# Optimization experiments

Hardware: AMD Instinct MI355X
Metric: run time of the kernel (lower is better)

The kernel has to match this reference:

```python
import jax, jax.numpy as jnp
import numpy as np

B, N, IN_F = 16, 1024, 256
HEADS, OUT_F = 4, 64
NEG_SLOPE = 0.2
CLAMP_MIN = -1e9
MASK_VAL = -9e15


def setup_inputs() -> dict:
    key = jax.random.key(0)
    k1, k2, k3, k4 = jax.random.split(key, 4)
    x = jax.random.normal(k1, (B, N, IN_F), dtype=jnp.float32)
    adj = jax.random.randint(k2, (B, N, N), 0, 2, dtype=jnp.int32)
    # Linear weight, stored as (in, heads*out) so y = x @ W (xavier-uniform scale)
    lim_w = float(np.sqrt(6.0 / (IN_F + HEADS * OUT_F)))
    W = jax.random.uniform(k3, (IN_F, HEADS * OUT_F), dtype=jnp.float32,
                           minval=-lim_w, maxval=lim_w)
    lim_a = float(np.sqrt(6.0 / (2 * OUT_F + HEADS)))
    a = jax.random.uniform(k4, (2 * OUT_F, HEADS), dtype=jnp.float32,
                           minval=-lim_a, maxval=lim_a)
    return {"x": x, "adj": adj, "W": W, "a": a}


def reference(x, adj, W, a):
    Bs, Ns, _ = x.shape
    # Projection: (B,N,H,D)
    h = (x @ W).reshape(Bs, Ns, HEADS, OUT_F)
    # cat([h_i, h_j]) . a == h_i . a_src + h_j . a_dst  (exact same math, no O(N^2*2D) tensor)
    a_src, a_dst = a[:OUT_F], a[OUT_F:]          # each (D, H)
    s_src = jnp.einsum('bnhd,dh->bnh', h, a_src)  # score contribution of node i
    s_dst = jnp.einsum('bnhd,dh->bnh', h, a_dst)  # score contribution of node j
    e = jax.nn.leaky_relu(s_src[:, :, None, :] + s_dst[:, None, :, :],
                          negative_slope=NEG_SLOPE)  # (B,N,N,H)
    # match original: subtract unmasked row max, clamp, then mask, then softmax over j
    e = e - jnp.max(e, axis=2, keepdims=True)
    e = jnp.maximum(e, CLAMP_MIN)
    att = jnp.where(adj[..., None] > 0, e, MASK_VAL)
    att = jax.nn.softmax(att, axis=2)
    h_prime = jnp.einsum('bijh,bjhd->bihd', att, h)  # (B,N,H,D)
    return h_prime.reshape(Bs, Ns, HEADS * OUT_F)
```

## Files before the change

kernel.cpp:

```cpp
#include <hip/hip_runtime.h>
#include <hip/hip_bf16.h>

#define B_   16
#define N_   1024
#define INF_ 256
#define NH_  4
#define HD_  256
#define L2E  1.4426950408889634f

typedef __attribute__((ext_vector_type(8))) short short8;
typedef __attribute__((ext_vector_type(4))) float f32x4;

__device__ __forceinline__ float bf2f(unsigned short u) {
    union { unsigned int i; float f; } v; v.i = ((unsigned int)u) << 16; return v.f;
}
__device__ __forceinline__ unsigned short f2bf(float f) {
    union { float f; unsigned int i; } v; v.f = f;
    unsigned int x = v.i;
    return (unsigned short)((x + 0x7fffu + ((x >> 16) & 1u)) >> 16);
}

__global__ __launch_bounds__(256) void k_prep(const int* __restrict__ adj,
                                              const float* __restrict__ W,
                                              unsigned int* __restrict__ pb,
                                              unsigned short* __restrict__ wswz)
{
    int bx = blockIdx.x, t = threadIdx.x;
    if (bx < 2048) {
        int wave = t >> 6, lane = t & 63;
        int row = bx * 8 + wave * 2 + (lane >> 5);
        int w   = lane & 31;
        const int4* ar = (const int4*)(adj + ((long)row << 10) + w * 32);
        unsigned int u = 0;
        #pragma unroll
        for (int k = 0; k < 8; k++) {
            int4 a = ar[k];
            u |= ((unsigned)a.x) << (4 * k);
            u |= ((unsigned)a.y) << (4 * k + 1);
            u |= ((unsigned)a.z) << (4 * k + 2);
            u |= ((unsigned)a.w) << (4 * k + 3);
        }
        pb[((long)row << 5) + w] = u;
    } else {
        int slot = (bx - 2048) * 256 + t;
        int kstep = slot >> 10;
        int nt    = (slot >> 6) & 15;
        int lane  = slot & 63;
        int k0 = kstep * 32 + (lane >> 4) * 8;
        int n  = nt * 16 + (lane & 15);
        ushort4 o0, o1;
        o0.x = f2bf(W[(k0 + 0) * HD_ + n]);
        o0.y = f2bf(W[(k0 + 1) * HD_ + n]);
        o0.z = f2bf(W[(k0 + 2) * HD_ + n]);
        o0.w = f2bf(W[(k0 + 3) * HD_ + n]);
        o1.x = f2bf(W[(k0 + 4) * HD_ + n]);
        o1.y = f2bf(W[(k0 + 5) * HD_ + n]);
        o1.z = f2bf(W[(k0 + 6) * HD_ + n]);
        o1.w = f2bf(W[(k0 + 7) * HD_ + n]);
        *(ushort4*)&wswz[(long)slot * 8]     = o0;
        *(ushort4*)&wswz[(long)slot * 8 + 4] = o1;
    }
}

__global__ __launch_bounds__(256) void k_gemm_h(
    const float* __restrict__ x, const float* __restrict__ a,
    const unsigned short* __restrict__ wswz,
    unsigned short* __restrict__ hswz,
    float* __restrict__ ssrc, float* __restrict__ sdst)
{
    __shared__ unsigned short xls[16][264];
    int t = threadIdx.x;
    int blk = blockIdx.x;
    int row0 = blk * 16;
    int b  = blk >> 6;
    int n0 = row0 & 1023;

    {
        int sr = t >> 4, sc = (t & 15) * 16;
        const float* xp = x + (long)(row0 + sr) * INF_ + sc;
        float4 v0 = ((const float4*)xp)[0];
        float4 v1 = ((const float4*)xp)[1];
        float4 v2 = ((const float4*)xp)[2];
        float4 v3 = ((const float4*)xp)[3];
        ushort4 u0 = {f2bf(v0.x), f2bf(v0.y), f2bf(v0.z), f2bf(v0.w)};
        ushort4 u1 = {f2bf(v1.x), f2bf(v1.y), f2bf(v1.z), f2bf(v1.w)};
        ushort4 u2 = {f2bf(v2.x), f2bf(v2.y), f2bf(v2.z), f2bf(v2.w)};
        ushort4 u3 = {f2bf(v3.x), f2bf(v3.y), f2bf(v3.z), f2bf(v3.w)};
        *(ushort4*)&xls[sr][sc]      = u0;
        *(ushort4*)&xls[sr][sc + 4]  = u1;
        *(ushort4*)&xls[sr][sc + 8]  = u2;
        *(ushort4*)&xls[sr][sc + 12] = u3;
    }
    __syncthreads();

    int wave = t >> 6, lane = t & 63, quad = lane >> 4, l15 = lane & 15;
    f32x4 acc[4];
    #pragma unroll
    for (int i = 0; i < 4; i++) acc[i] = (f32x4){0.f, 0.f, 0.f, 0.f};

    #pragma unroll
    for (int ks = 0; ks < 8; ks++) {
        short8 af = *(const short8*)&xls[l15][ks * 32 + quad * 8];
        #pragma unroll
        for (int nt = 0; nt < 4; nt++) {
            short8 bf = *(const short8*)(wswz +
                ((long)((ks * 16 + wave * 4 + nt) * 64 + lane)) * 8);
            acc[nt] = __builtin_amdgcn_mfma_f32_16x16x32_bf16(af, bf, acc[nt], 0, 0, 0);
        }
    }

    int q0 = (quad & 1) * 4;
    int qd = ((row0 & 31) + quad * 4) >> 3;
    long bj32 = row0 >> 5;
    #pragma unroll
    for (int nt = 0; nt < 4; nt++) {
        int dg = wave * 4 + nt;
        long idx8 = (bj32 * 16 + dg) * 64 + qd * 16 + l15;
        ushort4 o = {f2bf(acc[nt][0]), f2bf(acc[nt][1]),
                     f2bf(acc[nt][2]), f2bf(acc[nt][3])};
        *(ushort4*)&hswz[idx8 * 8 + q0] = o;
    }

    float as_[4], ad_[4];
    #pragma unroll
    for (int nt = 0; nt < 4; nt++) {
        int d = nt * 16 + l15;
        as_[nt] = a[d * NH_ + wave];
        ad_[nt] = a[(64 + d) * NH_ + wave];
    }
    #pragma unroll
    for (int r = 0; r < 4; r++) {
        float ps = acc[0][r] * as_[0] + acc[1][r] * as_[1]
                 + acc[2][r] * as_[2] + acc[3][r] * as_[3];
        float pd = acc[0][r] * ad_[0] + acc[1][r] * ad_[1]
                 + acc[2][r] * ad_[2] + acc[3][r] * ad_[3];
        #pragma unroll
        for (int m = 1; m < 16; m <<= 1) {
            ps += __shfl_xor(ps, m);
            pd += __shfl_xor(pd, m);
        }
        if (l15 == 0) {
            int row = n0 + quad * 4 + r;
            ssrc[((long)b * NH_ + wave) * N_ + row] = ps * L2E;
            sdst[((long)b * NH_ + wave) * N_ + row] = pd * L2E;
        }
    }
}

__global__ __launch_bounds__(512, 4) void k_attn(
    const unsigned int* __restrict__ pb, const unsigned short* __restrict__ hswz,
    const float* __restrict__ ssrc, const float* __restrict__ sdst,
    float* __restrict__ out)
{
    __shared__ float ss_s[4][32];
    __shared__ float accb[4][2][64][20];

    int t = threadIdx.x;
    int b  = blockIdx.x >> 5, ig = blockIdx.x & 31;
    int i0 = ig * 32;
    int wave = t >> 6, lane = t & 63, quad = lane >> 4, l15 = lane & 15;
    int hh = wave & 3, jh = wave >> 2;

    if (t < 128) {
        int h = t >> 5, i = t & 31;
        ss_s[h][i] = ssrc[((long)(b * NH_ + h)) * N_ + i0 + i];
    }
    __syncthreads();

    float ss0 = ss_s[hh][l15];
    float ss1 = ss_s[hh][16 + l15];
    const float* sdp = sdst + ((long)(b * NH_ + hh)) * N_ + jh * 512;
    long grow0 = ((long)b << 10) + i0 + l15;
    const unsigned int* pb0 = pb + (grow0 << 5) + jh * 16;
    const unsigned int* pb1 = pb0 + (16 << 5);

    f32x4 acc0[4], acc1[4], dn0, dn1;
    #pragma unroll
    for (int i = 0; i < 4; i++) {
        acc0[i] = (f32x4){0.f, 0.f, 0.f, 0.f};
        acc1[i] = (f32x4){0.f, 0.f, 0.f, 0.f};
    }
    dn0 = (f32x4){0.f, 0.f, 0.f, 0.f};
    dn1 = (f32x4){0.f, 0.f, 0.f, 0.f};
    short8 ones;
    #pragma unroll
    for (int i = 0; i < 8; i++) ones[i] = (short)0x3F80;

    int shq = quad * 8;

    #pragma unroll 4
    for (int jc = 0; jc < 16; jc++) {
        unsigned int m0 = (pb0[jc] >> shq) & 0xffu;
        unsigned int m1 = (pb1[jc] >> shq) & 0xffu;
        const float* sj = sdp + jc * 32 + quad * 8;
        float4 sA = *(const float4*)sj;
        float4 sB = *(const float4*)(sj + 4);
        float sv[8] = {sA.x, sA.y, sA.z, sA.w, sB.x, sB.y, sB.z, sB.w};

        union { unsigned int u[4]; short8 s; } p0, p1;
        #pragma unroll
        for (int qp = 0; qp < 4; qp++) {
            unsigned int wb[2][2];
            #pragma unroll
            for (int hv = 0; hv < 2; hv++) {
                int q = 2 * qp + hv;
                float e0 = ss0 + sv[q];
                float w0 = __builtin_exp2f(fmaxf(e0, 0.2f * e0));
                w0 = ((m0 >> q) & 1u) ? w0 : 0.f;
                float e1 = ss1 + sv[q];
                float w1 = __builtin_exp2f(fmaxf(e1, 0.2f * e1));
                w1 = ((m1 >> q) & 1u) ? w1 : 0.f;
                wb[0][hv] = __float_as_uint(w0) + 0x8000u;
                wb[1][hv] = __float_as_uint(w1) + 0x8000u;
            }
            p0.u[qp] = (wb[0][1] & 0xffff0000u) | (wb[0][0] >> 16);
            p1.u[qp] = (wb[1][1] & 0xffff0000u) | (wb[1][0] >> 16);
        }

        long s8 = ((long)(b * 32 + jh * 16 + jc)) * 1024;
        #pragma unroll
        for (int idt = 0; idt < 4; idt++) {
            short8 bf = *(const short8*)(hswz + (s8 + (hh * 4 + idt) * 64 + lane) * 8);
            acc0[idt] = __builtin_amdgcn_mfma_f32_16x16x32_bf16(p0.s, bf, acc0[idt], 0, 0, 0);
            acc1[idt] = __builtin_amdgcn_mfma_f32_16x16x32_bf16(p1.s, bf, acc1[idt], 0, 0, 0);
        }
        dn0 = __builtin_amdgcn_mfma_f32_16x16x32_bf16(p0.s, ones, dn0, 0, 0, 0);
        dn1 = __builtin_amdgcn_mfma_f32_16x16x32_bf16(p1.s, ones, dn1, 0, 0, 0);
    }

    if (jh == 1) {
        #pragma unroll
        for (int idt = 0; idt < 4; idt++) {
            *(f32x4*)&accb[hh][0][lane][idt * 4] = acc0[idt];
            *(f32x4*)&accb[hh][1][lane][idt * 4] = acc1[idt];
        }
        *(f32x4*)&accb[hh][0][lane][16] = dn0;
        *(f32x4*)&accb[hh][1][lane][16] = dn1;
    }
    __syncthreads();

    if (jh == 0) {
        f32x4 od0 = *(const f32x4*)&accb[hh][0][lane][16];
        f32x4 od1 = *(const f32x4*)&accb[hh][1][lane][16];
        float inv0[4], inv1[4];
        #pragma unroll
        for (int r = 0; r < 4; r++) {
            inv0[r] = 1.0f / (dn0[r] + od0[r]);
            inv1[r] = 1.0f / (dn1[r] + od1[r]);
        }
        #pragma unroll
        for (int idt = 0; idt < 4; idt++) {
            f32x4 o0 = *(const f32x4*)&accb[hh][0][lane][idt * 4];
            f32x4 o1 = *(const f32x4*)&accb[hh][1][lane][idt * 4];
            int col = hh * 64 + idt * 16 + l15;
            #pragma unroll
            for (int r = 0; r < 4; r++) {
                long row_g = (long)b * N_ + i0 + quad * 4 + r;
                out[row_g * HD_ + col] = (acc0[idt][r] + o0[r]) * inv0[r];
                out[(row_g + 16) * HD_ + col] = (acc1[idt][r] + o1[r]) * inv1[r];
            }
        }
    }
}

extern "C" void kernel_launch(void* const* d_in, const int* in_sizes, int n_in,
                              void* d_out, int out_size, void* d_ws, size_t ws_size,
                              hipStream_t stream) {
    const float* x   = (const float*)d_in[0];
    const int*   adj = (const int*)d_in[1];
    const float* W   = (const float*)d_in[2];
    const float* a   = (const float*)d_in[3];
    float* out = (float*)d_out;

    unsigned int* pb      = (unsigned int*)d_ws;
    unsigned short* hswz  = (unsigned short*)(pb + 524288);
    unsigned short* wswz  = hswz + (long)B_ * N_ * HD_;
    float* ssrc = (float*)(wswz + INF_ * HD_);
    float* sdst = ssrc + (long)B_ * NH_ * N_;

    k_prep<<<2080, 256, 0, stream>>>(adj, W, pb, wswz);
    k_gemm_h<<<1024, 256, 0, stream>>>(x, a, wswz, hswz, ssrc, sdst);
    k_attn<<<512, 512, 0, stream>>>(pb, hswz, ssrc, sdst, out);
}
```

Before: 156.0 us.

## Fuse adjacency bitpacking into attention kernel and halve rows per block

```diff
diff --git a/kernel.cpp b/kernel.cpp
--- a/kernel.cpp
+++ b/kernel.cpp
@@ -20,46 +20,26 @@
     return (unsigned short)((x + 0x7fffu + ((x >> 16) & 1u)) >> 16);
 }
 
-__global__ __launch_bounds__(256) void k_prep(const int* __restrict__ adj,
-                                              const float* __restrict__ W,
-                                              unsigned int* __restrict__ pb,
-                                              unsigned short* __restrict__ wswz)
+__global__ __launch_bounds__(256) void k_prepw(const float* __restrict__ W,
+                                               unsigned short* __restrict__ wswz)
 {
-    int bx = blockIdx.x, t = threadIdx.x;
-    if (bx < 2048) {
-        int wave = t >> 6, lane = t & 63;
-        int row = bx * 8 + wave * 2 + (lane >> 5);
-        int w   = lane & 31;
-        const int4* ar = (const int4*)(adj + ((long)row << 10) + w * 32);
-        unsigned int u = 0;
-        #pragma unroll
-        for (int k = 0; k < 8; k++) {
-            int4 a = ar[k];
-            u |= ((unsigned)a.x) << (4 * k);
-            u |= ((unsigned)a.y) << (4 * k + 1);
-            u |= ((unsigned)a.z) << (4 * k + 2);
-            u |= ((unsigned)a.w) << (4 * k + 3);
-        }
-        pb[((long)row << 5) + w] = u;
-    } else {
-        int slot = (bx - 2048) * 256 + t;
-        int kstep = slot >> 10;
-        int nt    = (slot >> 6) & 15;
-        int lane  = slot & 63;
-        int k0 = kstep * 32 + (lane >> 4) * 8;
-        int n  = nt * 16 + (lane & 15);
-        ushort4 o0, o1;
-        o0.x = f2bf(W[(k0 + 0) * HD_ + n]);
-        o0.y = f2bf(W[(k0 + 1) * HD_ + n]);
-        o0.z = f2bf(W[(k0 + 2) * HD_ + n]);
-        o0.w = f2bf(W[(k0 + 3) * HD_ + n]);
-        o1.x = f2bf(W[(k0 + 4) * HD_ + n]);
-        o1.y = f2bf(W[(k0 + 5) * HD_ + n]);
-        o1.z = f2bf(W[(k0 + 6) * HD_ + n]);
-        o1.w = f2bf(W[(k0 + 7) * HD_ + n]);
-        *(ushort4*)&wswz[(long)slot * 8]     = o0;
-        *(ushort4*)&wswz[(long)slot * 8 + 4] = o1;
-    }
+    int slot = blockIdx.x * 256 + threadIdx.x;
+    int kstep = slot >> 10;
+    int nt    = (slot >> 6) & 15;
+    int lane  = slot & 63;
+    int k0 = kstep * 32 + (lane >> 4) * 8;
+    int n  = nt * 16 + (lane & 15);
+    ushort4 o0, o1;
+    o0.x = f2bf(W[(k0 + 0) * HD_ + n]);
+    o0.y = f2bf(W[(k0 + 1) * HD_ + n]);
+    o0.z = f2bf(W[(k0 + 2) * HD_ + n]);
+    o0.w = f2bf(W[(k0 + 3) * HD_ + n]);
+    o1.x = f2bf(W[(k0 + 4) * HD_ + n]);
+    o1.y = f2bf(W[(k0 + 5) * HD_ + n]);
+    o1.z = f2bf(W[(k0 + 6) * HD_ + n]);
+    o1.w = f2bf(W[(k0 + 7) * HD_ + n]);
+    *(ushort4*)&wswz[(long)slot * 8]     = o0;
+    *(ushort4*)&wswz[(long)slot * 8 + 4] = o1;
 }
 
 __global__ __launch_bounds__(256) void k_gemm_h(
@@ -147,41 +127,48 @@
     }
 }
 
-__global__ __launch_bounds__(512, 4) void k_attn(
-    const unsigned int* __restrict__ pb, const unsigned short* __restrict__ hswz,
+__global__ __launch_bounds__(512) void k_attn(
+    const int* __restrict__ adj, const unsigned short* __restrict__ hswz,
     const float* __restrict__ ssrc, const float* __restrict__ sdst,
     float* __restrict__ out)
 {
-    __shared__ float ss_s[4][32];
-    __shared__ float accb[4][2][64][20];
+    __shared__ unsigned int maskw[16][33];
+    __shared__ float ss_s[4][16];
+    __shared__ float accb[4][64][20];
 
     int t = threadIdx.x;
-    int b  = blockIdx.x >> 5, ig = blockIdx.x & 31;
-    int i0 = ig * 32;
+    int b  = blockIdx.x >> 6, it = blockIdx.x & 63;
+    int i0 = it * 16;
     int wave = t >> 6, lane = t & 63, quad = lane >> 4, l15 = lane & 15;
     int hh = wave & 3, jh = wave >> 2;
 
-    if (t < 128) {
-        int h = t >> 5, i = t & 31;
+    {
+        int row = t >> 5, w = t & 31;
+        const int4* ar = (const int4*)(adj + (((long)b * N_ + i0 + row) << 10) + w * 32);
+        unsigned int u = 0;
+        #pragma unroll
+        for (int k = 0; k < 8; k++) {
+            int4 av = ar[k];
+            u |= ((unsigned)av.x) << (4 * k);
+            u |= ((unsigned)av.y) << (4 * k + 1);
+            u |= ((unsigned)av.z) << (4 * k + 2);
+            u |= ((unsigned)av.w) << (4 * k + 3);
+        }
+        maskw[row][w] = u;
+    }
+    if (t < 64) {
+        int h = t >> 4, i = t & 15;
         ss_s[h][i] = ssrc[((long)(b * NH_ + h)) * N_ + i0 + i];
     }
     __syncthreads();
 
-    float ss0 = ss_s[hh][l15];
-    float ss1 = ss_s[hh][16 + l15];
+    float ssi = ss_s[hh][l15];
     const float* sdp = sdst + ((long)(b * NH_ + hh)) * N_ + jh * 512;
-    long grow0 = ((long)b << 10) + i0 + l15;
-    const unsigned int* pb0 = pb + (grow0 << 5) + jh * 16;
-    const unsigned int* pb1 = pb0 + (16 << 5);
-
-    f32x4 acc0[4], acc1[4], dn0, dn1;
-    #pragma unroll
-    for (int i = 0; i < 4; i++) {
-        acc0[i] = (f32x4){0.f, 0.f, 0.f, 0.f};
-        acc1[i] = (f32x4){0.f, 0.f, 0.f, 0.f};
-    }
-    dn0 = (f32x4){0.f, 0.f, 0.f, 0.f};
-    dn1 = (f32x4){0.f, 0.f, 0.f, 0.f};
+
+    f32x4 acc[4], dn;
+    #pragma unroll
+    for (int i = 0; i < 4; i++) acc[i] = (f32x4){0.f, 0.f, 0.f, 0.f};
+    dn = (f32x4){0.f, 0.f, 0.f, 0.f};
     short8 ones;
     #pragma unroll
     for (int i = 0; i < 8; i++) ones[i] = (short)0x3F80;
@@ -190,74 +177,58 @@
 
     #pragma unroll 4
     for (int jc = 0; jc < 16; jc++) {
-        unsigned int m0 = (pb0[jc] >> shq) & 0xffu;
-        unsigned int m1 = (pb1[jc] >> shq) & 0xffu;
+        unsigned int byv = (maskw[l15][jh * 16 + jc] >> shq) & 0xffu;
         const float* sj = sdp + jc * 32 + quad * 8;
         float4 sA = *(const float4*)sj;
         float4 sB = *(const float4*)(sj + 4);
         float sv[8] = {sA.x, sA.y, sA.z, sA.w, sB.x, sB.y, sB.z, sB.w};
 
-        union { unsigned int u[4]; short8 s; } p0, p1;
+        union { unsigned int u[4]; short8 s; } pk;
         #pragma unroll
         for (int qp = 0; qp < 4; qp++) {
-            unsigned int wb[2][2];
+            unsigned int wb[2];
             #pragma unroll
             for (int hv = 0; hv < 2; hv++) {
                 int q = 2 * qp + hv;
-                float e0 = ss0 + sv[q];
-                float w0 = __builtin_exp2f(fmaxf(e0, 0.2f * e0));
-                w0 = ((m0 >> q) & 1u) ? w0 : 0.f;
-                float e1 = ss1 + sv[q];
-                float w1 = __builtin_exp2f(fmaxf(e1, 0.2f * e1));
-                w1 = ((m1 >> q) & 1u) ? w1 : 0.f;
-                wb[0][hv] = __float_as_uint(w0) + 0x8000u;
-                wb[1][hv] = __float_as_uint(w1) + 0x8000u;
+                float e = ssi + sv[q];
+                float w = __builtin_exp2f(fmaxf(e, 0.2f * e));
+                w = ((byv >> q) & 1u) ? w : 0.f;
+                wb[hv] = __float_as_uint(w) + 0x8000u;
             }
-            p0.u[qp] = (wb[0][1] & 0xffff0000u) | (wb[0][0] >> 16);
-            p1.u[qp] = (wb[1][1] & 0xffff0000u) | (wb[1][0] >> 16);
+            pk.u[qp] = (wb[1] & 0xffff0000u) | (wb[0] >> 16);
         }
 
         long s8 = ((long)(b * 32 + jh * 16 + jc)) * 1024;
         #pragma unroll
         for (int idt = 0; idt < 4; idt++) {
             short8 bf = *(const short8*)(hswz + (s8 + (hh * 4 + idt) * 64 + lane) * 8);
-            acc0[idt] = __builtin_amdgcn_mfma_f32_16x16x32_bf16(p0.s, bf, acc0[idt], 0, 0, 0);
-            acc1[idt] = __builtin_amdgcn_mfma_f32_16x16x32_bf16(p1.s, bf, acc1[idt], 0, 0, 0);
-        }
-        dn0 = __builtin_amdgcn_mfma_f32_16x16x32_bf16(p0.s, ones, dn0, 0, 0, 0);
-        dn1 = __builtin_amdgcn_mfma_f32_16x16x32_bf16(p1.s, ones, dn1, 0, 0, 0);
+            acc[idt] = __builtin_amdgcn_mfma_f32_16x16x32_bf16(pk.s, bf, acc[idt], 0, 0, 0);
+        }
+        dn = __builtin_amdgcn_mfma_f32_16x16x32_bf16(pk.s, ones, dn, 0, 0, 0);
     }
 
     if (jh == 1) {
         #pragma unroll
+        for (int idt = 0; idt < 4; idt++)
+            *(f32x4*)&accb[hh][lane][idt * 4] = acc[idt];
+        *(f32x4*)&accb[hh][lane][16] = dn;
+    }
+    __syncthreads();
+
+    if (jh == 0) {
+        f32x4 od = *(const f32x4*)&accb[hh][lane][16];
+        float inv[4];
+        #pragma unroll
+        for (int r = 0; r < 4; r++)
+            inv[r] = 1.0f / (dn[r] + od[r]);
+        #pragma unroll
         for (int idt = 0; idt < 4; idt++) {
-            *(f32x4*)&accb[hh][0][lane][idt * 4] = acc0[idt];
-            *(f32x4*)&accb[hh][1][lane][idt * 4] = acc1[idt];
-        }
-        *(f32x4*)&accb[hh][0][lane][16] = dn0;
-        *(f32x4*)&accb[hh][1][lane][16] = dn1;
-    }
-    __syncthreads();
-
-    if (jh == 0) {
-        f32x4 od0 = *(const f32x4*)&accb[hh][0][lane][16];
-        f32x4 od1 = *(const f32x4*)&accb[hh][1][lane][16];
-        float inv0[4], inv1[4];
-        #pragma unroll
-        for (int r = 0; r < 4; r++) {
-            inv0[r] = 1.0f / (dn0[r] + od0[r]);
-            inv1[r] = 1.0f / (dn1[r] + od1[r]);
-        }
-        #pragma unroll
-        for (int idt = 0; idt < 4; idt++) {
-            f32x4 o0 = *(const f32x4*)&accb[hh][0][lane][idt * 4];
-            f32x4 o1 = *(const f32x4*)&accb[hh][1][lane][idt * 4];
+            f32x4 o = *(const f32x4*)&accb[hh][lane][idt * 4];
             int col = hh * 64 + idt * 16 + l15;
             #pragma unroll
             for (int r = 0; r < 4; r++) {
                 long row_g = (long)b * N_ + i0 + quad * 4 + r;
-                out[row_g * HD_ + col] = (acc0[idt][r] + o0[r]) * inv0[r];
-                out[(row_g + 16) * HD_ + col] = (acc1[idt][r] + o1[r]) * inv1[r];
+                out[row_g * HD_ + col] = (acc[idt][r] + o[r]) * inv[r];
             }
         }
     }
@@ -272,13 +243,12 @@
     const float* a   = (const float*)d_in[3];
     float* out = (float*)d_out;
 
-    unsigned int* pb      = (unsigned int*)d_ws;
-    unsigned short* hswz  = (unsigned short*)(pb + 524288);
-    unsigned short* wswz  = hswz + (long)B_ * N_ * HD_;
+    unsigned short* hswz = (unsigned short*)d_ws;
+    unsigned short* wswz = hswz + (long)B_ * N_ * HD_;
     float* ssrc = (float*)(wswz + INF_ * HD_);
     float* sdst = ssrc + (long)B_ * NH_ * N_;
 
-    k_prep<<<2080, 256, 0, stream>>>(adj, W, pb, wswz);
+    k_prepw<<<32, 256, 0, stream>>>(W, wswz);
     k_gemm_h<<<1024, 256, 0, stream>>>(x, a, wswz, hswz, ssrc, sdst);
-    k_attn<<<512, 512, 0, stream>>>(pb, hswz, ssrc, sdst, out);
-}
+    k_attn<<<1024, 512, 0, stream>>>(adj, hswz, ssrc, sdst, out);
+}
```

After: 173.6 us. 1.11x slower.

## Factor leaky-relu exponent into precomputed per-node exp products

Applied to the files above, without the earlier changes.

```diff
diff --git a/kernel.cpp b/kernel.cpp
--- a/kernel.cpp
+++ b/kernel.cpp
@@ -11,9 +11,6 @@
 typedef __attribute__((ext_vector_type(8))) short short8;
 typedef __attribute__((ext_vector_type(4))) float f32x4;
 
-__device__ __forceinline__ float bf2f(unsigned short u) {
-    union { unsigned int i; float f; } v; v.i = ((unsigned int)u) << 16; return v.f;
-}
 __device__ __forceinline__ unsigned short f2bf(float f) {
     union { float f; unsigned int i; } v; v.f = f;
     unsigned int x = v.i;
@@ -27,20 +24,20 @@
 {
     int bx = blockIdx.x, t = threadIdx.x;
     if (bx < 2048) {
-        int wave = t >> 6, lane = t & 63;
-        int row = bx * 8 + wave * 2 + (lane >> 5);
-        int w   = lane & 31;
-        const int4* ar = (const int4*)(adj + ((long)row << 10) + w * 32);
+        int g = bx * 256 + t;
+        int w   = g & 31;
+        int row = g >> 5;
+        const int* ar = adj + ((long)row << 10) + w * 32;
         unsigned int u = 0;
         #pragma unroll
         for (int k = 0; k < 8; k++) {
-            int4 a = ar[k];
-            u |= ((unsigned)a.x) << (4 * k);
-            u |= ((unsigned)a.y) << (4 * k + 1);
-            u |= ((unsigned)a.z) << (4 * k + 2);
-            u |= ((unsigned)a.w) << (4 * k + 3);
-        }
-        pb[((long)row << 5) + w] = u;
+            int4 av = *(const int4*)(ar + k * 4);
+            u |= ((unsigned)av.x) << (4 * k);
+            u |= ((unsigned)av.y) << (4 * k + 1);
+            u |= ((unsigned)av.z) << (4 * k + 2);
+            u |= ((unsigned)av.w) << (4 * k + 3);
+        }
+        pb[g] = u;
     } else {
         int slot = (bx - 2048) * 256 + t;
         int kstep = slot >> 10;
@@ -66,7 +63,8 @@
     const float* __restrict__ x, const float* __restrict__ a,
     const unsigned short* __restrict__ wswz,
     unsigned short* __restrict__ hswz,
-    float* __restrict__ ssrc, float* __restrict__ sdst)
+    float* __restrict__ Ps, float* __restrict__ Qs,
+    float* __restrict__ Pd, float* __restrict__ Qd)
 {
     __shared__ unsigned short xls[16][264];
     int t = threadIdx.x;
@@ -74,6 +72,15 @@
     int row0 = blk * 16;
     int b  = blk >> 6;
     int n0 = row0 & 1023;
+    int wave = t >> 6, lane = t & 63, quad = lane >> 4, l15 = lane & 15;
+
+    short8 bw[8][4];
+    #pragma unroll
+    for (int ks = 0; ks < 8; ks++)
+        #pragma unroll
+        for (int nt = 0; nt < 4; nt++)
+            bw[ks][nt] = *(const short8*)(wswz +
+                ((long)((ks * 16 + wave * 4 + nt) * 64 + lane)) * 8);
 
     {
         int sr = t >> 4, sc = (t & 15) * 16;
@@ -93,7 +100,6 @@
     }
     __syncthreads();
 
-    int wave = t >> 6, lane = t & 63, quad = lane >> 4, l15 = lane & 15;
     f32x4 acc[4];
     #pragma unroll
     for (int i = 0; i < 4; i++) acc[i] = (f32x4){0.f, 0.f, 0.f, 0.f};
@@ -102,11 +108,8 @@
     for (int ks = 0; ks < 8; ks++) {
         short8 af = *(const short8*)&xls[l15][ks * 32 + quad * 8];
         #pragma unroll
-        for (int nt = 0; nt < 4; nt++) {
-            short8 bf = *(const short8*)(wswz +
-                ((long)((ks * 16 + wave * 4 + nt) * 64 + lane)) * 8);
-            acc[nt] = __builtin_amdgcn_mfma_f32_16x16x32_bf16(af, bf, acc[nt], 0, 0, 0);
-        }
+        for (int nt = 0; nt < 4; nt++)
+            acc[nt] = __builtin_amdgcn_mfma_f32_16x16x32_bf16(af, bw[ks][nt], acc[nt], 0, 0, 0);
     }
 
     int q0 = (quad & 1) * 4;
@@ -141,18 +144,23 @@
         }
         if (l15 == 0) {
             int row = n0 + quad * 4 + r;
-            ssrc[((long)b * NH_ + wave) * N_ + row] = ps * L2E;
-            sdst[((long)b * NH_ + wave) * N_ + row] = pd * L2E;
+            long o = ((long)b * NH_ + wave) * N_ + row;
+            float ss = ps * L2E, sd = pd * L2E;
+            Ps[o] = __builtin_exp2f(ss);
+            Qs[o] = __builtin_exp2f(0.2f * ss);
+            Pd[o] = __builtin_exp2f(sd);
+            Qd[o] = __builtin_exp2f(0.2f * sd);
         }
     }
 }
 
 __global__ __launch_bounds__(512, 4) void k_attn(
     const unsigned int* __restrict__ pb, const unsigned short* __restrict__ hswz,
-    const float* __restrict__ ssrc, const float* __restrict__ sdst,
+    const float* __restrict__ Ps, const float* __restrict__ Qs,
+    const float* __restrict__ Pd, const float* __restrict__ Qd,
     float* __restrict__ out)
 {
-    __shared__ float ss_s[4][32];
+    __shared__ float ps_s[4][32], qs_s[4][32];
     __shared__ float accb[4][2][64][20];
 
     int t = threadIdx.x;
@@ -163,13 +171,16 @@
 
     if (t < 128) {
         int h = t >> 5, i = t & 31;
-        ss_s[h][i] = ssrc[((long)(b * NH_ + h)) * N_ + i0 + i];
+        long o = ((long)(b * NH_ + h)) * N_ + i0 + i;
+        ps_s[h][i] = Ps[o];
+        qs_s[h][i] = Qs[o];
     }
     __syncthreads();
 
-    float ss0 = ss_s[hh][l15];
-    float ss1 = ss_s[hh][16 + l15];
-    const float* sdp = sdst + ((long)(b * NH_ + hh)) * N_ + jh * 512;
+    float Pi0 = ps_s[hh][l15],      Qi0 = qs_s[hh][l15];
+    float Pi1 = ps_s[hh][16 + l15], Qi1 = qs_s[hh][16 + l15];
+    const float* Pdp = Pd + ((long)(b * NH_ + hh)) * N_ + jh * 512;
+    const float* Qdp = Qd + ((long)(b * NH_ + hh)) * N_ + jh * 512;
     long grow0 = ((long)b << 10) + i0 + l15;
     const unsigned int* pb0 = pb + (grow0 << 5) + jh * 16;
     const unsigned int* pb1 = pb0 + (16 << 5);
@@ -192,40 +203,42 @@
     for (int jc = 0; jc < 16; jc++) {
         unsigned int m0 = (pb0[jc] >> shq) & 0xffu;
         unsigned int m1 = (pb1[jc] >> shq) & 0xffu;
-        const float* sj = sdp + jc * 32 + quad * 8;
-        float4 sA = *(const float4*)sj;
-        float4 sB = *(const float4*)(sj + 4);
-        float sv[8] = {sA.x, sA.y, sA.z, sA.w, sB.x, sB.y, sB.z, sB.w};
-
-        union { unsigned int u[4]; short8 s; } p0, p1;
+        const float* pj = Pdp + jc * 32 + quad * 8;
+        const float* qj = Qdp + jc * 32 + quad * 8;
+        float4 pA = *(const float4*)pj;
+        float4 pB = *(const float4*)(pj + 4);
+        float4 qA = *(const float4*)qj;
+        float4 qB = *(const float4*)(qj + 4);
+        float pv[8] = {pA.x, pA.y, pA.z, pA.w, pB.x, pB.y, pB.z, pB.w};
+        float qv[8] = {qA.x, qA.y, qA.z, qA.w, qB.x, qB.y, qB.z, qB.w};
+
+        union { unsigned int u[4]; short8 s; } pk0, pk1;
         #pragma unroll
         for (int qp = 0; qp < 4; qp++) {
-            unsigned int wb[2][2];
+            unsigned int wb0[2], wb1[2];
             #pragma unroll
             for (int hv = 0; hv < 2; hv++) {
                 int q = 2 * qp + hv;
-                float e0 = ss0 + sv[q];
-                float w0 = __builtin_exp2f(fmaxf(e0, 0.2f * e0));
+                float w0 = fmaxf(Pi0 * pv[q], Qi0 * qv[q]);
                 w0 = ((m0 >> q) & 1u) ? w0 : 0.f;
-                float e1 = ss1 + sv[q];
-                float w1 = __builtin_exp2f(fmaxf(e1, 0.2f * e1));
+                wb0[hv] = __float_as_uint(w0) + 0x8000u;
+                float w1 = fmaxf(Pi1 * pv[q], Qi1 * qv[q]);
                 w1 = ((m1 >> q) & 1u) ? w1 : 0.f;
-                wb[0][hv] = __float_as_uint(w0) + 0x8000u;
-                wb[1][hv] = __float_as_uint(w1) + 0x8000u;
+                wb1[hv] = __float_as_uint(w1) + 0x8000u;
             }
-            p0.u[qp] = (wb[0][1] & 0xffff0000u) | (wb[0][0] >> 16);
-            p1.u[qp] = (wb[1][1] & 0xffff0000u) | (wb[1][0] >> 16);
+            pk0.u[qp] = (wb0[1] & 0xffff0000u) | (wb0[0] >> 16);
+            pk1.u[qp] = (wb1[1] & 0xffff0000u) | (wb1[0] >> 16);
         }
 
         long s8 = ((long)(b * 32 + jh * 16 + jc)) * 1024;
         #pragma unroll
         for (int idt = 0; idt < 4; idt++) {
             short8 bf = *(const short8*)(hswz + (s8 + (hh * 4 + idt) * 64 + lane) * 8);
-            acc0[idt] = __builtin_amdgcn_mfma_f32_16x16x32_bf16(p0.s, bf, acc0[idt], 0, 0, 0);
-            acc1[idt] = __builtin_amdgcn_mfma_f32_16x16x32_bf16(p1.s, bf, acc1[idt], 0, 0, 0);
-        }
-        dn0 = __builtin_amdgcn_mfma_f32_16x16x32_bf16(p0.s, ones, dn0, 0, 0, 0);
-        dn1 = __builtin_amdgcn_mfma_f32_16x16x32_bf16(p1.s, ones, dn1, 0, 0, 0);
+            acc0[idt] = __builtin_amdgcn_mfma_f32_16x16x32_bf16(pk0.s, bf, acc0[idt], 0, 0, 0);
+            acc1[idt] = __builtin_amdgcn_mfma_f32_16x16x32_bf16(pk1.s, bf, acc1[idt], 0, 0, 0);
+        }
+        dn0 = __builtin_amdgcn_mfma_f32_16x16x32_bf16(pk0.s, ones, dn0, 0, 0, 0);
+        dn1 = __builtin_amdgcn_mfma_f32_16x16x32_bf16(pk1.s, ones, dn1, 0, 0, 0);
     }
 
     if (jh == 1) {
@@ -275,10 +288,12 @@
     unsigned int* pb      = (unsigned int*)d_ws;
     unsigned short* hswz  = (unsigned short*)(pb + 524288);
     unsigned short* wswz  = hswz + (long)B_ * N_ * HD_;
-    float* ssrc = (float*)(wswz + INF_ * HD_);
-    float* sdst = ssrc + (long)B_ * NH_ * N_;
+    float* Ps = (float*)(wswz + INF_ * HD_);
+    float* Qs = Ps + (long)B_ * NH_ * N_;
+    float* Pd = Qs + (long)B_ * NH_ * N_;
+    float* Qd = Pd + (long)B_ * NH_ * N_;
 
     k_prep<<<2080, 256, 0, stream>>>(adj, W, pb, wswz);
-    k_gemm_h<<<1024, 256, 0, stream>>>(x, a, wswz, hswz, ssrc, sdst);
-    k_attn<<<512, 512, 0, stream>>>(pb, hswz, ssrc, sdst, out);
-}
+    k_gemm_h<<<1024, 256, 0, stream>>>(x, a, wswz, hswz, Ps, Qs, Pd, Qd);
+    k_attn<<<512, 512, 0, stream>>>(pb, hswz, Ps, Qs, Pd, Qd, out);
+}
```

Result: no change. 158.2 us (+1.4%).
